# Optimization experiments

Measured on AMD Instinct MI355X. Metric: run time of the kernel, lower is better.

Reference implementation:

```python
import jax, jax.numpy as jnp
import numpy as np

CH = [344, 352, 686, 679, 1246, 973]  # int(128*3*0.8984), etc.


def binarize(x):
    # sign forward, hardtanh STE backward (standard 1W1A binarization)
    cl = jnp.clip(x, -1.0, 1.0)
    return cl + jax.lax.stop_gradient(jnp.sign(x) - cl)


def bconv(x, w):
    # BinarizeConv2d: conv(sign(x), sign(w)), 3x3, stride 1, pad 1, no bias
    return jax.lax.conv_general_dilated(
        binarize(x), binarize(w), (1, 1), ((1, 1), (1, 1)),
        dimension_numbers=("NCHW", "OIHW", "NCHW"))


def bn(x, p, eps=1e-5):
    # p: [4, C] stacked (gamma, beta, running_mean, running_var), inference BN
    g, b, m, v = p[0], p[1], p[2], p[3]
    scale = (g * jax.lax.rsqrt(v + eps))[None, :, None, None]
    return (x - m[None, :, None, None]) * scale + b[None, :, None, None]


def pool(x):
    return jax.lax.reduce_window(x, -jnp.inf, jax.lax.max,
                                 (1, 1, 2, 2), (1, 1, 2, 2), "VALID")


def htanh(x):
    return jnp.clip(x, -1.0, 1.0)


def setup_inputs() -> dict:
    key = jax.random.key(0)
    ks = jax.random.split(key, 20)
    x = jax.random.normal(ks[0], (256, 3, 32, 32), jnp.float32)
    chs = [3] + CH
    out = {"x": x}
    for i in range(6):
        n = 3 * 3 * chs[i + 1]
        w = jax.random.normal(ks[1 + i], (chs[i + 1], chs[i], 3, 3), jnp.float32) * np.sqrt(2.0 / n).astype(np.float32)
        out[f"w{i}"] = w
        g = jnp.ones((chs[i + 1],), jnp.float32)
        b = jnp.zeros((chs[i + 1],), jnp.float32)
        m = jax.random.normal(ks[7 + i], (chs[i + 1],), jnp.float32) * 0.1
        v = jax.random.uniform(ks[13 + i], (chs[i + 1],), jnp.float32) * 0.5 + 0.5
        out[f"p{i}"] = jnp.stack([g, b, m, v])
    out["fcw"] = jax.random.normal(ks[19], (10, 15568), jnp.float32) * 0.01
    out["fcb"] = jnp.zeros((10,), jnp.float32)
    return out


def reference(x, w0, w1, w2, w3, w4, w5, p0, p1, p2, p3, p4, p5, fcw, fcb):
    x = htanh(bn(bconv(x, w0), p0))          # [B,344,32,32]
    x = htanh(bn(pool(bconv(x, w1)), p1))    # [B,352,16,16]
    x = htanh(bn(bconv(x, w2), p2))          # [B,686,16,16]
    x = htanh(bn(pool(bconv(x, w3)), p3))    # [B,679,8,8]
    x = htanh(bn(bconv(x, w4), p4))          # [B,1246,8,8]
    x = htanh(bn(pool(bconv(x, w5)), p5))    # [B,973,4,4]
    x = x.reshape(x.shape[0], -1)            # [B,15568]
    return binarize(x) @ binarize(fcw).T + fcb
```

## Files before the change

### kernel.cpp

```cpp
#include <hip/hip_runtime.h>
#include <stdint.h>

typedef unsigned long long u64;
typedef int v4i  __attribute__((ext_vector_type(4)));
typedef int v8i  __attribute__((ext_vector_type(8)));
typedef float v16f __attribute__((ext_vector_type(16)));

static __device__ __forceinline__ v16f mfma_fp4(v4i a, v4i b, v16f c) {
    v8i A, B;
    A[0] = a[0]; A[1] = a[1]; A[2] = a[2]; A[3] = a[3];
    A[4] = a[0]; A[5] = a[1]; A[6] = a[2]; A[7] = a[3];
    B[0] = b[0]; B[1] = b[1]; B[2] = b[2]; B[3] = b[3];
    B[4] = b[0]; B[5] = b[1]; B[6] = b[2]; B[7] = b[3];
    return __builtin_amdgcn_mfma_scale_f32_32x32x64_f8f6f4(
        A, B, c, 4, 4, 0, 0x7F7F7F7F, 0, 0x7F7F7F7F);
}

static __device__ __forceinline__ void gload_lds16(const void* g, void* l) {
    __builtin_amdgcn_global_load_lds(
        (const __attribute__((address_space(1))) unsigned int*)g,
        (__attribute__((address_space(3))) unsigned int*)l, 16, 0, 0);
}

__global__ void pack_input_kernel(const float* __restrict__ x, u64* __restrict__ a0)
{
    int idx = blockIdx.x * blockDim.x + threadIdx.x;
    if (idx >= 256 * 1024) return;
    int b = idx >> 10, pix = idx & 1023;
    const float* xp = x + (size_t)b * 3072 + pix;
    u64 wd = 0;
    if (xp[0]    > 0.f) wd |= 1ull;
    if (xp[1024] > 0.f) wd |= 2ull;
    if (xp[2048] > 0.f) wd |= 4ull;
    a0[idx] = wd;
}

__global__ void pack_w_fp4(const float* __restrict__ w, unsigned* __restrict__ wb,
                           int O, int C, int KWIN, int OCG)
{
    int idx = blockIdx.x * blockDim.x + threadIdx.x;
    int total = 9 * KWIN * OCG * 64;
    if (idx >= total) return;
    int lane = idx & 63;
    int rest = idx >> 6;
    int og = rest % OCG; rest /= OCG;
    int c64 = rest % KWIN; int t = rest / KWIN;
    int oc = og * 32 + (lane & 31);
    int h = lane >> 5;
    unsigned out[4];
#pragma unroll
    for (int d = 0; d < 4; ++d) {
        unsigned dw = 0;
#pragma unroll
        for (int j = 0; j < 8; ++j) {
            int c = c64 * 64 + h * 32 + d * 8 + ((j >> 1) + (j & 1) * 4);
            unsigned nib = 0;
            if (oc < O && c < C)
                nib = (w[(size_t)(oc * C + c) * 9 + t] > 0.f) ? 0x2u : 0xAu;
            dw |= nib << (4 * j);
        }
        out[d] = dw;
    }
    *(v4i*)(wb + (size_t)idx * 4) = *(v4i*)out;
}

__global__ void pack_bn_kernel(const float* __restrict__ p, float* __restrict__ sa,
                               float* __restrict__ sb, int C)
{
    int i = blockIdx.x * blockDim.x + threadIdx.x;
    if (i >= C) return;
    float g = p[i], b = p[C + i], m = p[2 * C + i], v = p[3 * C + i];
    float s = g * rsqrtf(v + 1e-5f);
    sa[i] = s;
    sb[i] = fmaf(-m, s, b);
}

__global__ void pack_fc_kernel(const float* __restrict__ fcw, u64* __restrict__ wfc)
{
    int idx = blockIdx.x * blockDim.x + threadIdx.x;
    if (idx >= 10 * 256) return;
    int w = idx & 15;
    int p = (idx >> 4) & 15;
    int k = idx >> 8;
    u64 word = 0;
    for (int c2 = 0; c2 < 64; ++c2) {
        int c = w * 64 + c2;
        if (c < 973) {
            if (fcw[(size_t)k * 15568 + c * 16 + p] > 0.f) word |= (1ull << c2);
        }
    }
    wfc[idx] = word;
}

static __device__ __forceinline__ v4i fp4_unpack32(unsigned wh)
{
    v4i r;
#pragma unroll
    for (int d = 0; d < 4; ++d) {
        unsigned b = (wh >> (8 * d)) & 0xffu;
        unsigned lo = ((b & 0xFu) * 0x00204081u) & 0x01010101u;
        unsigned hi = ((b >> 4)   * 0x00204081u) & 0x01010101u;
        unsigned spread = lo | (hi << 4);
        r[d] = (int)(0xAAAAAAAAu - (spread << 3));
    }
    return r;
}

template <int H, int W, int TH, int TW, int NIMG, int KWIN, int OCG_T, int OCW,
          int COUT, bool POOL>
__global__ __launch_bounds__(256, 2)
void conv_v6f(const u64* __restrict__ act, const char* __restrict__ wb,
              const float* __restrict__ sA, const float* __restrict__ sB,
              u64* __restrict__ outp)
{
    constexpr int CW = TW + 2;
    constexpr int CELLS_I = (TH + 2) * CW;
    constexpr int CELLS = NIMG * CELLS_I;
    constexpr int PLANE = CELLS * 16;
    constexpr int BSZ = 18432;
    constexpr size_t NPX  = (size_t)256 * H * W;
    constexpr size_t NPXO = POOL ? ((size_t)256 * (H / 2) * (W / 2))
                                 : ((size_t)256 * H * W);
    __shared__ __attribute__((aligned(16))) char smem[BSZ + 2 * PLANE];

    const int tid  = threadIdx.x;
    const int lane = tid & 63;
    const int wm   = tid >> 6;
    const int h    = lane >> 5;
    const int m    = lane & 31;

    int b0i, y0;
    if constexpr (NIMG == 1) {
        b0i = blockIdx.x >> 1;
        y0 = (blockIdx.x & 1) * TH;
    } else {
        b0i = blockIdx.x * NIMG;
        y0 = 0;
    }

    const int ocg0 = blockIdx.y * 2;
    const int gw   = blockIdx.y;

    int aoff[4];
#pragma unroll
    for (int ag = 0; ag < 4; ++ag) {
        int p = wm * 128 + ag * 32 + m;
        int img = p / (TH * TW);
        int pp = p % (TH * TW);
        aoff[ag] = ((img * CELLS_I + (pp / TW) * CW + (pp % TW)) << 4) + h * PLANE;
    }

    v16f acc[4][2];
#pragma unroll
    for (int ag = 0; ag < 4; ++ag)
#pragma unroll
        for (int o = 0; o < 2; ++o)
#pragma unroll
            for (int i = 0; i < 16; ++i) acc[ag][o][i] = 0.0f;

#pragma unroll 1
    for (int c64 = 0; c64 < KWIN; ++c64) {
        for (int u = wm; u < 18; u += 4) {
            int og = u & 1, t = u >> 1;
            const char* gp = wb + ((size_t)((t * KWIN + c64) * OCG_T + ocg0 + og)) * 1024
                             + lane * 16;
            gload_lds16(gp, smem + u * 1024);
        }
        for (int cell = tid; cell < CELLS; cell += 256) {
            int img, c2;
            if constexpr (NIMG == 1) { img = 0; c2 = cell; }
            else { img = cell / CELLS_I; c2 = cell % CELLS_I; }
            int cy = c2 / CW, cx = c2 % CW;
            int gy = y0 + cy - 1, gx = cx - 1;
            char* dst = smem + BSZ + cell * 16;
            if ((unsigned)gy < (unsigned)H && (unsigned)gx < (unsigned)W) {
                u64 wd = act[(size_t)c64 * NPX
                             + (size_t)(b0i + img) * (H * W) + gy * W + gx];
                *(v4i*)dst           = fp4_unpack32((unsigned)wd);
                *(v4i*)(dst + PLANE) = fp4_unpack32((unsigned)(wd >> 32));
            } else {
                v4i z = {0, 0, 0, 0};
                *(v4i*)dst           = z;
                *(v4i*)(dst + PLANE) = z;
            }
        }
        __syncthreads();

#pragma unroll
        for (int t = 0; t < 9; ++t) {
            const int aimm = BSZ + (((t / 3) * CW) + (t % 3)) * 16;
            v4i b0 = *(const v4i*)(smem + (t * 2 + 0) * 1024 + lane * 16);
            v4i b1 = *(const v4i*)(smem + (t * 2 + 1) * 1024 + lane * 16);
            v4i a0 = *(const v4i*)(smem + aoff[0] + aimm);
            v4i a1 = *(const v4i*)(smem + aoff[1] + aimm);
            v4i a2 = *(const v4i*)(smem + aoff[2] + aimm);
            v4i a3 = *(const v4i*)(smem + aoff[3] + aimm);
            acc[0][0] = mfma_fp4(a0, b0, acc[0][0]);
            acc[1][0] = mfma_fp4(a1, b0, acc[1][0]);
            acc[2][0] = mfma_fp4(a2, b0, acc[2][0]);
            acc[3][0] = mfma_fp4(a3, b0, acc[3][0]);
            acc[0][1] = mfma_fp4(a0, b1, acc[0][1]);
            acc[1][1] = mfma_fp4(a1, b1, acc[1][1]);
            acc[2][1] = mfma_fp4(a2, b1, acc[2][1]);
            acc[3][1] = mfma_fp4(a3, b1, acc[3][1]);
        }
        __syncthreads();
    }

    const int ocA = ocg0 * 32 + m;
    const int ocB = ocA + 32;
    const float fa0 = sA[ocA < COUT ? ocA : 0], fb0 = sB[ocA < COUT ? ocA : 0];
    const float fa1 = sA[ocB < COUT ? ocB : 0], fb1 = sB[ocB < COUT ? ocB : 0];
    u64* outg = outp + (size_t)gw * NPXO;

#pragma unroll
    for (int ag = 0; ag < 4; ++ag) {
        if constexpr (POOL && TW == 32) {
            if (ag & 1) continue;
#pragma unroll
            for (int gi = 0; gi < 8; ++gi) {
                const int g = gi * 2;
                float v0 = fmaxf(fmaxf(acc[ag][0][g], acc[ag][0][g ^ 1]),
                                 fmaxf(acc[ag + 1][0][g], acc[ag + 1][0][g ^ 1]));
                float v1 = fmaxf(fmaxf(acc[ag][1][g], acc[ag][1][g ^ 1]),
                                 fmaxf(acc[ag + 1][1][g], acc[ag + 1][1][g ^ 1]));
                u64 bal0 = __ballot((ocA < COUT) && (fmaf(v0, fa0, fb0) > 0.f));
                u64 bal1 = __ballot((ocB < COUT) && (fmaf(v1, fa1, fb1) > 0.f));
                u64 w_lo = (bal0 & 0xffffffffull) | (bal1 << 32);
                u64 w_hi = (bal0 >> 32) | (bal1 & 0xffffffff00000000ull);
                int pyo  = wm * 2 + (ag >> 1);
                int pxo0 = ((g & 3) >> 1) + 4 * (g >> 2);
                size_t rowb = ((size_t)b0i * (H / 2) + (y0 / 2 + pyo)) * (W / 2);
                if (lane == (ag >> 1) * 16 + gi * 2)
                    outg[rowb + pxo0] = w_lo;
                else if (lane == (ag >> 1) * 16 + gi * 2 + 1)
                    outg[rowb + pxo0 + 2] = w_hi;
            }
        } else if constexpr (POOL) {
#pragma unroll
            for (int gi = 0; gi < 4; ++gi) {
                const int g = gi * 2;
                float v0 = fmaxf(fmaxf(acc[ag][0][g], acc[ag][0][g ^ 1]),
                                 fmaxf(acc[ag][0][g ^ 8], acc[ag][0][(g ^ 8) | 1]));
                float v1 = fmaxf(fmaxf(acc[ag][1][g], acc[ag][1][g ^ 1]),
                                 fmaxf(acc[ag][1][g ^ 8], acc[ag][1][(g ^ 8) | 1]));
                u64 bal0 = __ballot((ocA < COUT) && (fmaf(v0, fa0, fb0) > 0.f));
                u64 bal1 = __ballot((ocB < COUT) && (fmaf(v1, fa1, fb1) > 0.f));
                u64 w_lo = (bal0 & 0xffffffffull) | (bal1 << 32);
                u64 w_hi = (bal0 >> 32) | (bal1 & 0xffffffff00000000ull);
                int img  = wm >> 1;
                int pyo  = (wm & 1) * 4 + ag;
                int pxo0 = ((g >> 1) & 1) | (((g >> 2) & 1) << 2);
                size_t rowb = ((size_t)(b0i + img) * (TH / 2) + pyo) * (TW / 2);
                if (lane == (ag * 4 + gi) * 2)
                    outg[rowb + pxo0] = w_lo;
                else if (lane == (ag * 4 + gi) * 2 + 1)
                    outg[rowb + pxo0 + 2] = w_hi;
            }
        } else {
#pragma unroll
            for (int reg = 0; reg < 16; ++reg) {
                u64 bal0 = __ballot((ocA < COUT) && (fmaf(acc[ag][0][reg], fa0, fb0) > 0.f));
                u64 bal1 = __ballot((ocB < COUT) && (fmaf(acc[ag][1][reg], fa1, fb1) > 0.f));
                u64 w_lo = (bal0 & 0xffffffffull) | (bal1 << 32);
                u64 w_hi = (bal0 >> 32) | (bal1 & 0xffffffff00000000ull);
                int row  = (reg & 3) + 8 * (reg >> 2);
                int p_lo = wm * 128 + ag * 32 + row;
                int p_hi = p_lo + 4;
                if (lane == reg * 2) {
                    int img, py, px;
                    if constexpr (TW == 32) { img = 0; py = p_lo >> 5; px = p_lo & 31; }
                    else { img = p_lo >> 8; py = (p_lo >> 4) & 15; px = p_lo & 15; }
                    outg[((size_t)(b0i + img) * H + (y0 + py)) * W + px] = w_lo;
                } else if (lane == reg * 2 + 1) {
                    int img, py, px;
                    if constexpr (TW == 32) { img = 0; py = p_hi >> 5; px = p_hi & 31; }
                    else { img = p_hi >> 8; py = (p_hi >> 4) & 15; px = p_hi & 15; }
                    outg[((size_t)(b0i + img) * H + (y0 + py)) * W + px] = w_hi;
                }
            }
        }
    }
}

template <int KWIN, int OCG, int OCW, int COUT, bool POOL>
__global__ __launch_bounds__(256, 3)
void conv_m8f(const u64* __restrict__ act, const char* __restrict__ wb,
              const float* __restrict__ sA, const float* __restrict__ sB,
              u64* __restrict__ outp)
{
    constexpr int CELLS = 100;
    constexpr int PLANE = CELLS * 16;
    constexpr int IMG = 2 * PLANE;
    constexpr int NPX8 = 16384;
    constexpr size_t NPXO = POOL ? 4096 : 16384;
    __shared__ __attribute__((aligned(16))) char smem[4 * IMG];

    const int tid  = threadIdx.x;
    const int lane = tid & 63;
    const int wave = tid >> 6;
    const int h    = lane >> 5;
    const int m    = lane & 31;

    const int b = blockIdx.x * 4 + wave;
    const int ocg0 = blockIdx.y * 2;
    const int gw = blockIdx.y;

    int aoff[2];
#pragma unroll
    for (int ph = 0; ph < 2; ++ph) {
        int p = ph * 32 + m;
        aoff[ph] = wave * IMG + ((p >> 3) * 10 + (p & 7)) * 16 + h * PLANE;
    }

    v16f acc[2][2];
#pragma unroll
    for (int a = 0; a < 2; ++a)
#pragma unroll
        for (int o = 0; o < 2; ++o)
#pragma unroll
            for (int i = 0; i < 16; ++i) acc[a][o][i] = 0.0f;

    const u64* actb = act + (size_t)b * 64;

    v4i b0n, b1n;
    {
        const v4i* pn = (const v4i*)(wb + ((size_t)ocg0) * 1024) + lane;
        b0n = pn[0]; b1n = pn[64];
    }

#pragma unroll 1
    for (int c64 = 0; c64 < KWIN; ++c64) {
        for (int cell = lane; cell < CELLS; cell += 64) {
            int cy = cell / 10, cx = cell % 10;
            int gy = cy - 1, gx = cx - 1;
            char* dst = smem + wave * IMG + cell * 16;
            if ((unsigned)gy < 8u && (unsigned)gx < 8u) {
                u64 wd = actb[(size_t)c64 * NPX8 + (gy * 8 + gx)];
                *(v4i*)dst           = fp4_unpack32((unsigned)wd);
                *(v4i*)(dst + PLANE) = fp4_unpack32((unsigned)(wd >> 32));
            } else {
                v4i z = {0, 0, 0, 0};
                *(v4i*)dst           = z;
                *(v4i*)(dst + PLANE) = z;
            }
        }
        __syncthreads();

#pragma unroll
        for (int t = 0; t < 9; ++t) {
            v4i b0 = b0n, b1 = b1n;
            {
                const int tn = (t + 1) % 9;
                const int cn = (t == 8) ? (c64 + 1) : c64;
                const v4i* pn = (const v4i*)(wb + ((size_t)((tn * KWIN + cn) * OCG + ocg0)) * 1024) + lane;
                b0n = pn[0]; b1n = pn[64];
            }
            const int toff = ((t / 3) * 10 + (t % 3)) * 16;
            v4i a0 = *(const v4i*)(smem + aoff[0] + toff);
            v4i a1 = *(const v4i*)(smem + aoff[1] + toff);
            acc[0][0] = mfma_fp4(a0, b0, acc[0][0]);
            acc[1][0] = mfma_fp4(a1, b0, acc[1][0]);
            acc[0][1] = mfma_fp4(a0, b1, acc[0][1]);
            acc[1][1] = mfma_fp4(a1, b1, acc[1][1]);
        }
        __syncthreads();
    }

    const int ocA = ocg0 * 32 + m;
    const int ocB = ocA + 32;
    const float fa0 = sA[ocA < COUT ? ocA : 0], fb0 = sB[ocA < COUT ? ocA : 0];
    const float fa1 = sA[ocB < COUT ? ocB : 0], fb1 = sB[ocB < COUT ? ocB : 0];
    u64* outg = outp + (size_t)gw * NPXO;

#pragma unroll
    for (int ph = 0; ph < 2; ++ph) {
        if constexpr (POOL) {
#pragma unroll
            for (int gi = 0; gi < 4; ++gi) {
                const int g = (gi & 1) * 2 + (gi >> 1) * 8;
                float v0 = fmaxf(fmaxf(acc[ph][0][g], acc[ph][0][g ^ 1]),
                                 fmaxf(acc[ph][0][g ^ 4], acc[ph][0][(g ^ 4) | 1]));
                float v1 = fmaxf(fmaxf(acc[ph][1][g], acc[ph][1][g ^ 1]),
                                 fmaxf(acc[ph][1][g ^ 4], acc[ph][1][(g ^ 4) | 1]));
                u64 bal0 = __ballot((ocA < COUT) && (fmaf(v0, fa0, fb0) > 0.f));
                u64 bal1 = __ballot((ocB < COUT) && (fmaf(v1, fa1, fb1) > 0.f));
                u64 w_lo = (bal0 & 0xffffffffull) | (bal1 << 32);
                u64 w_hi = (bal0 >> 32) | (bal1 & 0xffffffff00000000ull);
                int pyo  = ph * 2 + ((g >> 3) & 1);
                int pxo0 = (g >> 1) & 1;
                int pxo1 = pxo0 | 2;
                size_t rowb = ((size_t)b * 4 + pyo) * 4;
                if (lane == (ph * 4 + gi) * 2)
                    outg[rowb + pxo0] = w_lo;
                else if (lane == (ph * 4 + gi) * 2 + 1)
                    outg[rowb + pxo1] = w_hi;
            }
        } else {
#pragma unroll
            for (int reg = 0; reg < 16; ++reg) {
                u64 bal0 = __ballot((ocA < COUT) && (fmaf(acc[ph][0][reg], fa0, fb0) > 0.f));
                u64 bal1 = __ballot((ocB < COUT) && (fmaf(acc[ph][1][reg], fa1, fb1) > 0.f));
                u64 w_lo = (bal0 & 0xffffffffull) | (bal1 << 32);
                u64 w_hi = (bal0 >> 32) | (bal1 & 0xffffffff00000000ull);
                int row  = (reg & 3) + 8 * (reg >> 2);
                int p_lo = ph * 32 + row;
                int p_hi = p_lo + 4;
                if (lane == reg * 2)
                    outg[((size_t)b * 8 + (p_lo >> 3)) * 8 + (p_lo & 7)] = w_lo;
                else if (lane == reg * 2 + 1)
                    outg[((size_t)b * 8 + (p_hi >> 3)) * 8 + (p_hi & 7)] = w_hi;
            }
        }
    }
}

__global__ void fc_kernel(const u64* __restrict__ a6, const u64* __restrict__ wfc,
                          const float* __restrict__ fcb, float* __restrict__ out)
{
    int idx = blockIdx.x * blockDim.x + threadIdx.x;
    if (idx >= 2560) return;
    int k = idx % 10, b = idx / 10;
    const u64* wq = wfc + (size_t)k * 256;
    int pop = 0;
#pragma unroll 8
    for (int q = 0; q < 256; ++q) {
        int w = q & 15, p = q >> 4;
        pop += __popcll(a6[(size_t)w * 4096 + b * 16 + p] ^ wq[q]);
    }
    out[idx] = (float)(15568 - 2 * pop) + fcb[k];
}

extern "C" void kernel_launch(void* const* d_in, const int* in_sizes, int n_in,
                              void* d_out, int out_size, void* d_ws, size_t ws_size,
                              hipStream_t stream)
{
    const float* x   = (const float*)d_in[0];
    const float* w0  = (const float*)d_in[1];
    const float* p0  = (const float*)d_in[2];
    const float* w1  = (const float*)d_in[3];
    const float* p1  = (const float*)d_in[4];
    const float* w2  = (const float*)d_in[5];
    const float* p2  = (const float*)d_in[6];
    const float* w3  = (const float*)d_in[7];
    const float* p3  = (const float*)d_in[8];
    const float* w4  = (const float*)d_in[9];
    const float* p4  = (const float*)d_in[10];
    const float* w5  = (const float*)d_in[11];
    const float* p5  = (const float*)d_in[12];
    const float* fcw = (const float*)d_in[13];
    const float* fcb = (const float*)d_in[14];
    float* out = (float*)d_out;

    u64* WS = (u64*)d_ws;
    u64* A0 = WS;
    u64* A1 = A0 + 262144;
    u64* A2 = A1 + 1572864;
    u64* A3 = A2 + 393216;
    u64* A4 = A3 + 720896;
    u64* A5 = A4 + 180224;
    u64* A6 = A5 + 327680;
    u64* WFp = A6 + 65536;
    char* WB0 = (char*)(WFp + 2560);
    char* WB1 = WB0 + 110592;
    char* WB2 = WB1 + 663552;
    char* WB3 = WB2 + 1327104;
    char* WB4 = WB3 + 2433024;
    char* WB5 = WB4 + 4055040;
    float* SA0 = (float*)(WB5 + 5898240);
    float* SB0 = SA0 + 1280;
    float* SA1 = SB0 + 1280;
    float* SB1 = SA1 + 1280;
    float* SA2 = SB1 + 1280;
    float* SB2 = SA2 + 1280;
    float* SA3 = SB2 + 1280;
    float* SB3 = SA3 + 1280;
    float* SA4 = SB3 + 1280;
    float* SB4 = SA4 + 1280;
    float* SA5 = SB4 + 1280;
    float* SB5 = SA5 + 1280;

    pack_input_kernel<<<1024, 256, 0, stream>>>(x, A0);
    pack_w_fp4<<<(9 * 1 * 12 * 64 + 255) / 256, 256, 0, stream>>>(w0, (unsigned*)WB0, 344, 3, 1, 12);
    pack_w_fp4<<<(9 * 6 * 12 * 64 + 255) / 256, 256, 0, stream>>>(w1, (unsigned*)WB1, 352, 344, 6, 12);
    pack_w_fp4<<<(9 * 6 * 24 * 64 + 255) / 256, 256, 0, stream>>>(w2, (unsigned*)WB2, 686, 352, 6, 24);
    pack_w_fp4<<<(9 * 11 * 24 * 64 + 255) / 256, 256, 0, stream>>>(w3, (unsigned*)WB3, 679, 686, 11, 24);
    pack_w_fp4<<<(9 * 11 * 40 * 64 + 255) / 256, 256, 0, stream>>>(w4, (unsigned*)WB4, 1246, 679, 11, 40);
    pack_w_fp4<<<(9 * 20 * 32 * 64 + 255) / 256, 256, 0, stream>>>(w5, (unsigned*)WB5, 973, 1246, 20, 32);
    pack_bn_kernel<<<2, 256, 0, stream>>>(p0, SA0, SB0, 344);
    pack_bn_kernel<<<2, 256, 0, stream>>>(p1, SA1, SB1, 352);
    pack_bn_kernel<<<3, 256, 0, stream>>>(p2, SA2, SB2, 686);
    pack_bn_kernel<<<3, 256, 0, stream>>>(p3, SA3, SB3, 679);
    pack_bn_kernel<<<5, 256, 0, stream>>>(p4, SA4, SB4, 1246);
    pack_bn_kernel<<<4, 256, 0, stream>>>(p5, SA5, SB5, 973);
    pack_fc_kernel<<<10, 256, 0, stream>>>(fcw, WFp);

    conv_v6f<32, 32, 16, 32, 1,  1, 12,  6, 344, false>
        <<<dim3(512, 6), 256, 0, stream>>>(A0, WB0, SA0, SB0, A1);
    conv_v6f<32, 32, 16, 32, 1,  6, 12,  6, 352, true>
        <<<dim3(512, 6), 256, 0, stream>>>(A1, WB1, SA1, SB1, A2);
    conv_v6f<16, 16, 16, 16, 2,  6, 24, 11, 686, false>
        <<<dim3(128, 11), 256, 0, stream>>>(A2, WB2, SA2, SB2, A3);
    conv_v6f<16, 16, 16, 16, 2, 11, 24, 11, 679, true>
        <<<dim3(128, 11), 256, 0, stream>>>(A3, WB3, SA3, SB3, A4);
    conv_m8f<11, 40, 20, 1246, false>
        <<<dim3(64, 20), 256, 0, stream>>>(A4, WB4, SA4, SB4, A5);
    conv_m8f<20, 32, 16, 973, true>
        <<<dim3(64, 16), 256, 0, stream>>>(A5, WB5, SA5, SB5, A6);

    fc_kernel<<<10, 256, 0, stream>>>(A6, WFp, fcb, out);
}
```

Before: 938.0 us.

## Double-buffer weight and activation LDS tiles in binary conv main loop

Splits the per-K-window LDS staging into two buffers so the next window's weights (async global_load_lds) and activations (register prefetch then unpack) load while the current window's MFMAs run. Cell coordinates and halo zero-fill are now computed once up front instead of every iteration. This hides global load latency and drops one barrier per iteration, at the cost of roughly doubled LDS usage, which may lower occupancy under launch_bounds(256,2), plus extra prefetch registers.

```diff
diff --git a/kernel.cpp b/kernel.cpp
--- a/kernel.cpp
+++ b/kernel.cpp
@@ -118,10 +118,13 @@
     constexpr int CELLS = NIMG * CELLS_I;
     constexpr int PLANE = CELLS * 16;
     constexpr int BSZ = 18432;
+    constexpr int DB = (KWIN > 1) ? 2 : 1;
+    constexpr int ABASE = DB * BSZ;
+    constexpr int NCELL = (CELLS + 255) / 256;
     constexpr size_t NPX  = (size_t)256 * H * W;
     constexpr size_t NPXO = POOL ? ((size_t)256 * (H / 2) * (W / 2))
                                  : ((size_t)256 * H * W);
-    __shared__ __attribute__((aligned(16))) char smem[BSZ + 2 * PLANE];
+    __shared__ __attribute__((aligned(16))) char smem[ABASE + DB * 2 * PLANE];
 
     const int tid  = threadIdx.x;
     const int lane = tid & 63;
@@ -150,51 +153,86 @@
         aoff[ag] = ((img * CELLS_I + (pp / TW) * CW + (pp % TW)) << 4) + h * PLANE;
     }
 
-    v16f acc[4][2];
-#pragma unroll
-    for (int ag = 0; ag < 4; ++ag)
-#pragma unroll
-        for (int o = 0; o < 2; ++o)
-#pragma unroll
-            for (int i = 0; i < 16; ++i) acc[ag][o][i] = 0.0f;
-
-#pragma unroll 1
-    for (int c64 = 0; c64 < KWIN; ++c64) {
-        for (int u = wm; u < 18; u += 4) {
-            int og = u & 1, t = u >> 1;
-            const char* gp = wb + ((size_t)((t * KWIN + c64) * OCG_T + ocg0 + og)) * 1024
-                             + lane * 16;
-            gload_lds16(gp, smem + u * 1024);
-        }
-        for (int cell = tid; cell < CELLS; cell += 256) {
+    int cpx[NCELL];
+    int coff[NCELL];
+#pragma unroll
+    for (int i = 0; i < NCELL; ++i) {
+        int cell = tid + i * 256;
+        cpx[i] = -1; coff[i] = 0;
+        if (cell < CELLS) {
             int img, c2;
             if constexpr (NIMG == 1) { img = 0; c2 = cell; }
             else { img = cell / CELLS_I; c2 = cell % CELLS_I; }
             int cy = c2 / CW, cx = c2 % CW;
             int gy = y0 + cy - 1, gx = cx - 1;
-            char* dst = smem + BSZ + cell * 16;
+            coff[i] = cell * 16;
             if ((unsigned)gy < (unsigned)H && (unsigned)gx < (unsigned)W) {
-                u64 wd = act[(size_t)c64 * NPX
-                             + (size_t)(b0i + img) * (H * W) + gy * W + gx];
-                *(v4i*)dst           = fp4_unpack32((unsigned)wd);
-                *(v4i*)(dst + PLANE) = fp4_unpack32((unsigned)(wd >> 32));
+                cpx[i] = (b0i + img) * (H * W) + gy * W + gx;
             } else {
                 v4i z = {0, 0, 0, 0};
-                *(v4i*)dst           = z;
-                *(v4i*)(dst + PLANE) = z;
-            }
-        }
-        __syncthreads();
+                char* d0 = smem + ABASE + coff[i];
+                *(v4i*)d0           = z;
+                *(v4i*)(d0 + PLANE) = z;
+                if constexpr (DB == 2) {
+                    *(v4i*)(d0 + 2 * PLANE) = z;
+                    *(v4i*)(d0 + 3 * PLANE) = z;
+                }
+            }
+        }
+    }
+
+    for (int u = wm; u < 18; u += 4) {
+        int og = u & 1, t = u >> 1;
+        const char* gp = wb + ((size_t)((t * KWIN) * OCG_T + ocg0 + og)) * 1024
+                         + lane * 16;
+        gload_lds16(gp, smem + u * 1024);
+    }
+#pragma unroll
+    for (int i = 0; i < NCELL; ++i) if (cpx[i] >= 0) {
+        u64 wd = act[cpx[i]];
+        char* dst = smem + ABASE + coff[i];
+        *(v4i*)dst           = fp4_unpack32((unsigned)wd);
+        *(v4i*)(dst + PLANE) = fp4_unpack32((unsigned)(wd >> 32));
+    }
+    __syncthreads();
+
+    v16f acc[4][2];
+#pragma unroll
+    for (int ag = 0; ag < 4; ++ag)
+#pragma unroll
+        for (int o = 0; o < 2; ++o)
+#pragma unroll
+            for (int i = 0; i < 16; ++i) acc[ag][o][i] = 0.0f;
+
+#pragma unroll 1
+    for (int c64 = 0; c64 < KWIN; ++c64) {
+        const bool more = (c64 + 1 < KWIN);
+
+        u64 wdn[NCELL];
+        if (more) {
+#pragma unroll
+            for (int i = 0; i < NCELL; ++i)
+                wdn[i] = (cpx[i] >= 0) ? act[(size_t)(c64 + 1) * NPX + cpx[i]] : 0;
+            for (int u = wm; u < 18; u += 4) {
+                int og = u & 1, t = u >> 1;
+                const char* gp = wb + ((size_t)((t * KWIN + (c64 + 1)) * OCG_T + ocg0 + og)) * 1024
+                                 + lane * 16;
+                gload_lds16(gp, smem + ((c64 + 1) & 1) * BSZ + u * 1024);
+            }
+        }
+
+        const char* bb = smem + ((DB == 2) ? (c64 & 1) * BSZ : 0);
+        const char* ab = smem + ABASE + ((DB == 2) ? (c64 & 1) * (2 * PLANE) : 0);
 
 #pragma unroll
         for (int t = 0; t < 9; ++t) {
-            const int aimm = BSZ + (((t / 3) * CW) + (t % 3)) * 16;
-            v4i b0 = *(const v4i*)(smem + (t * 2 + 0) * 1024 + lane * 16);
-            v4i b1 = *(const v4i*)(smem + (t * 2 + 1) * 1024 + lane * 16);
-            v4i a0 = *(const v4i*)(smem + aoff[0] + aimm);
-            v4i a1 = *(const v4i*)(smem + aoff[1] + aimm);
-            v4i a2 = *(const v4i*)(smem + aoff[2] + aimm);
-            v4i a3 = *(const v4i*)(smem + aoff[3] + aimm);
+            const int aimm = (((t / 3) * CW) + (t % 3)) * 16;
+            v4i b0 = *(const v4i*)(bb + (t * 2 + 0) * 1024 + lane * 16);
+            v4i b1 = *(const v4i*)(bb + (t * 2 + 1) * 1024 + lane * 16);
+            v4i a0 = *(const v4i*)(ab + aoff[0] + aimm);
+            v4i a1 = *(const v4i*)(ab + aoff[1] + aimm);
+            v4i a2 = *(const v4i*)(ab + aoff[2] + aimm);
+            v4i a3 = *(const v4i*)(ab + aoff[3] + aimm);
             acc[0][0] = mfma_fp4(a0, b0, acc[0][0]);
             acc[1][0] = mfma_fp4(a1, b0, acc[1][0]);
             acc[2][0] = mfma_fp4(a2, b0, acc[2][0]);
@@ -204,7 +242,17 @@
             acc[2][1] = mfma_fp4(a2, b1, acc[2][1]);
             acc[3][1] = mfma_fp4(a3, b1, acc[3][1]);
         }
-        __syncthreads();
+
+        if (more) {
+            char* an = smem + ABASE + (((c64 + 1) & 1) * (2 * PLANE));
+#pragma unroll
+            for (int i = 0; i < NCELL; ++i) if (cpx[i] >= 0) {
+                char* dst = an + coff[i];
+                *(v4i*)dst           = fp4_unpack32((unsigned)wdn[i]);
+                *(v4i*)(dst + PLANE) = fp4_unpack32((unsigned)(wdn[i] >> 32));
+            }
+            __syncthreads();
+        }
     }
 
     const int ocA = ocg0 * 32 + m;
```

New measurement: 1.932 ms. 106% more time.

## Route 8x8 layers through the generic conv kernel with multi-image tiles

Applied to the files above, without the earlier changes.

Removes the specialized conv_m8f kernel for the two 8x8 layers and instead instantiates the generic conv_v6f kernel with 8x8 tiles covering 8 images per block. New TW==8 epilogue paths are added for pooled and unpooled output indexing. The grid shrinks from 64 to 32 blocks along the batch dimension, and each block's weight fragments are reused across more pixels. This lowers weight reloads per output but reduces parallelism and may change occupancy or LDS use.

```diff
diff --git a/kernel.cpp b/kernel.cpp
--- a/kernel.cpp
+++ b/kernel.cpp
@@ -235,6 +235,27 @@
                     outg[rowb + pxo0] = w_lo;
                 else if (lane == (ag >> 1) * 16 + gi * 2 + 1)
                     outg[rowb + pxo0 + 2] = w_hi;
+            }
+        } else if constexpr (POOL && TW == 8) {
+#pragma unroll
+            for (int gi = 0; gi < 4; ++gi) {
+                const int g = (gi & 1) * 2 + (gi >> 1) * 8;
+                float v0 = fmaxf(fmaxf(acc[ag][0][g], acc[ag][0][g ^ 1]),
+                                 fmaxf(acc[ag][0][g ^ 4], acc[ag][0][(g ^ 4) | 1]));
+                float v1 = fmaxf(fmaxf(acc[ag][1][g], acc[ag][1][g ^ 1]),
+                                 fmaxf(acc[ag][1][g ^ 4], acc[ag][1][(g ^ 4) | 1]));
+                u64 bal0 = __ballot((ocA < COUT) && (fmaf(v0, fa0, fb0) > 0.f));
+                u64 bal1 = __ballot((ocB < COUT) && (fmaf(v1, fa1, fb1) > 0.f));
+                u64 w_lo = (bal0 & 0xffffffffull) | (bal1 << 32);
+                u64 w_hi = (bal0 >> 32) | (bal1 & 0xffffffff00000000ull);
+                int img  = wm * 2 + (ag >> 1);
+                int opy  = (ag & 1) * 2 + (g >> 3);
+                int opx0 = (g >> 1) & 1;
+                size_t rowb = ((size_t)(b0i + img) * 4 + opy) * 4;
+                if (lane == (ag * 4 + gi) * 2)
+                    outg[rowb + opx0] = w_lo;
+                else if (lane == (ag * 4 + gi) * 2 + 1)
+                    outg[rowb + opx0 + 2] = w_hi;
             }
         } else if constexpr (POOL) {
 #pragma unroll
@@ -270,146 +291,16 @@
                 if (lane == reg * 2) {
                     int img, py, px;
                     if constexpr (TW == 32) { img = 0; py = p_lo >> 5; px = p_lo & 31; }
+                    else if constexpr (TW == 8) { img = p_lo >> 6; py = (p_lo >> 3) & 7; px = p_lo & 7; }
                     else { img = p_lo >> 8; py = (p_lo >> 4) & 15; px = p_lo & 15; }
                     outg[((size_t)(b0i + img) * H + (y0 + py)) * W + px] = w_lo;
                 } else if (lane == reg * 2 + 1) {
                     int img, py, px;
                     if constexpr (TW == 32) { img = 0; py = p_hi >> 5; px = p_hi & 31; }
+                    else if constexpr (TW == 8) { img = p_hi >> 6; py = (p_hi >> 3) & 7; px = p_hi & 7; }
                     else { img = p_hi >> 8; py = (p_hi >> 4) & 15; px = p_hi & 15; }
                     outg[((size_t)(b0i + img) * H + (y0 + py)) * W + px] = w_hi;
                 }
-            }
-        }
-    }
-}
-
-template <int KWIN, int OCG, int OCW, int COUT, bool POOL>
-__global__ __launch_bounds__(256, 3)
-void conv_m8f(const u64* __restrict__ act, const char* __restrict__ wb,
-              const float* __restrict__ sA, const float* __restrict__ sB,
-              u64* __restrict__ outp)
-{
-    constexpr int CELLS = 100;
-    constexpr int PLANE = CELLS * 16;
-    constexpr int IMG = 2 * PLANE;
-    constexpr int NPX8 = 16384;
-    constexpr size_t NPXO = POOL ? 4096 : 16384;
-    __shared__ __attribute__((aligned(16))) char smem[4 * IMG];
-
-    const int tid  = threadIdx.x;
-    const int lane = tid & 63;
-    const int wave = tid >> 6;
-    const int h    = lane >> 5;
-    const int m    = lane & 31;
-
-    const int b = blockIdx.x * 4 + wave;
-    const int ocg0 = blockIdx.y * 2;
-    const int gw = blockIdx.y;
-
-    int aoff[2];
-#pragma unroll
-    for (int ph = 0; ph < 2; ++ph) {
-        int p = ph * 32 + m;
-        aoff[ph] = wave * IMG + ((p >> 3) * 10 + (p & 7)) * 16 + h * PLANE;
-    }
-
-    v16f acc[2][2];
-#pragma unroll
-    for (int a = 0; a < 2; ++a)
-#pragma unroll
-        for (int o = 0; o < 2; ++o)
-#pragma unroll
-            for (int i = 0; i < 16; ++i) acc[a][o][i] = 0.0f;
-
-    const u64* actb = act + (size_t)b * 64;
-
-    v4i b0n, b1n;
-    {
-        const v4i* pn = (const v4i*)(wb + ((size_t)ocg0) * 1024) + lane;
-        b0n = pn[0]; b1n = pn[64];
-    }
-
-#pragma unroll 1
-    for (int c64 = 0; c64 < KWIN; ++c64) {
-        for (int cell = lane; cell < CELLS; cell += 64) {
-            int cy = cell / 10, cx = cell % 10;
-            int gy = cy - 1, gx = cx - 1;
-            char* dst = smem + wave * IMG + cell * 16;
-            if ((unsigned)gy < 8u && (unsigned)gx < 8u) {
-                u64 wd = actb[(size_t)c64 * NPX8 + (gy * 8 + gx)];
-                *(v4i*)dst           = fp4_unpack32((unsigned)wd);
-                *(v4i*)(dst + PLANE) = fp4_unpack32((unsigned)(wd >> 32));
-            } else {
-                v4i z = {0, 0, 0, 0};
-                *(v4i*)dst           = z;
-                *(v4i*)(dst + PLANE) = z;
-            }
-        }
-        __syncthreads();
-
-#pragma unroll
-        for (int t = 0; t < 9; ++t) {
-            v4i b0 = b0n, b1 = b1n;
-            {
-                const int tn = (t + 1) % 9;
-                const int cn = (t == 8) ? (c64 + 1) : c64;
-                const v4i* pn = (const v4i*)(wb + ((size_t)((tn * KWIN + cn) * OCG + ocg0)) * 1024) + lane;
-                b0n = pn[0]; b1n = pn[64];
-            }
-            const int toff = ((t / 3) * 10 + (t % 3)) * 16;
-            v4i a0 = *(const v4i*)(smem + aoff[0] + toff);
-            v4i a1 = *(const v4i*)(smem + aoff[1] + toff);
-            acc[0][0] = mfma_fp4(a0, b0, acc[0][0]);
-            acc[1][0] = mfma_fp4(a1, b0, acc[1][0]);
-            acc[0][1] = mfma_fp4(a0, b1, acc[0][1]);
-            acc[1][1] = mfma_fp4(a1, b1, acc[1][1]);
-        }
-        __syncthreads();
-    }
-
-    const int ocA = ocg0 * 32 + m;
-    const int ocB = ocA + 32;
-    const float fa0 = sA[ocA < COUT ? ocA : 0], fb0 = sB[ocA < COUT ? ocA : 0];
-    const float fa1 = sA[ocB < COUT ? ocB : 0], fb1 = sB[ocB < COUT ? ocB : 0];
-    u64* outg = outp + (size_t)gw * NPXO;
-
-#pragma unroll
-    for (int ph = 0; ph < 2; ++ph) {
-        if constexpr (POOL) {
-#pragma unroll
-            for (int gi = 0; gi < 4; ++gi) {
-                const int g = (gi & 1) * 2 + (gi >> 1) * 8;
-                float v0 = fmaxf(fmaxf(acc[ph][0][g], acc[ph][0][g ^ 1]),
-                                 fmaxf(acc[ph][0][g ^ 4], acc[ph][0][(g ^ 4) | 1]));
-                float v1 = fmaxf(fmaxf(acc[ph][1][g], acc[ph][1][g ^ 1]),
-                                 fmaxf(acc[ph][1][g ^ 4], acc[ph][1][(g ^ 4) | 1]));
-                u64 bal0 = __ballot((ocA < COUT) && (fmaf(v0, fa0, fb0) > 0.f));
-                u64 bal1 = __ballot((ocB < COUT) && (fmaf(v1, fa1, fb1) > 0.f));
-                u64 w_lo = (bal0 & 0xffffffffull) | (bal1 << 32);
-                u64 w_hi = (bal0 >> 32) | (bal1 & 0xffffffff00000000ull);
-                int pyo  = ph * 2 + ((g >> 3) & 1);
-                int pxo0 = (g >> 1) & 1;
-                int pxo1 = pxo0 | 2;
-                size_t rowb = ((size_t)b * 4 + pyo) * 4;
-                if (lane == (ph * 4 + gi) * 2)
-                    outg[rowb + pxo0] = w_lo;
-                else if (lane == (ph * 4 + gi) * 2 + 1)
-                    outg[rowb + pxo1] = w_hi;
-            }
-        } else {
-#pragma unroll
-            for (int reg = 0; reg < 16; ++reg) {
-                u64 bal0 = __ballot((ocA < COUT) && (fmaf(acc[ph][0][reg], fa0, fb0) > 0.f));
-                u64 bal1 = __ballot((ocB < COUT) && (fmaf(acc[ph][1][reg], fa1, fb1) > 0.f));
-                u64 w_lo = (bal0 & 0xffffffffull) | (bal1 << 32);
-                u64 w_hi = (bal0 >> 32) | (bal1 & 0xffffffff00000000ull);
-                int row  = (reg & 3) + 8 * (reg >> 2);
-                int p_lo = ph * 32 + row;
-                int p_hi = p_lo + 4;
-                if (lane == reg * 2)
-                    outg[((size_t)b * 8 + (p_lo >> 3)) * 8 + (p_lo & 7)] = w_lo;
-                else if (lane == reg * 2 + 1)
-                    outg[((size_t)b * 8 + (p_hi >> 3)) * 8 + (p_hi & 7)] = w_hi;
             }
         }
     }
@@ -503,10 +394,10 @@
         <<<dim3(128, 11), 256, 0, stream>>>(A2, WB2, SA2, SB2, A3);
     conv_v6f<16, 16, 16, 16, 2, 11, 24, 11, 679, true>
         <<<dim3(128, 11), 256, 0, stream>>>(A3, WB3, SA3, SB3, A4);
-    conv_m8f<11, 40, 20, 1246, false>
-        <<<dim3(64, 20), 256, 0, stream>>>(A4, WB4, SA4, SB4, A5);
-    conv_m8f<20, 32, 16, 973, true>
-        <<<dim3(64, 16), 256, 0, stream>>>(A5, WB5, SA5, SB5, A6);
+    conv_v6f< 8,  8,  8,  8, 8, 11, 40, 20, 1246, false>
+        <<<dim3(32, 20), 256, 0, stream>>>(A4, WB4, SA4, SB4, A5);
+    conv_v6f< 8,  8,  8,  8, 8, 20, 32, 16, 973, true>
+        <<<dim3(32, 16), 256, 0, stream>>>(A5, WB5, SA5, SB5, A6);
 
     fc_kernel<<<10, 256, 0, stream>>>(A6, WFp, fcb, out);
 }
```

Result: slower. 959.3 us (+2.3%).
